# Optimization experiments

Hardware: AMD Instinct MI355X
Metric: run time of the kernel (lower is better)

The kernel has to match this reference:

```python
import jax, jax.numpy as jnp
import numpy as np

B, S, DM, H, HD = 2, 2048, 1024, 16, 64
MEM_SIZE = 1000
K_SIMILAR, K_CONTIG = 8, 2
K_TOTAL = K_SIMILAR + K_CONTIG  # 10 memory tokens
NEG = -1e9


def setup_inputs() -> dict:
    key = jax.random.key(0)
    k1, k2, k3, k4, k5, k6 = jax.random.split(key, 6)
    inputs = jax.random.normal(k1, (B, S, DM), dtype=jnp.float32)
    attention_mask = jnp.ones((B, S), dtype=jnp.float32)
    Wq = jax.random.normal(k2, (DM, H * HD), dtype=jnp.float32) * 0.02
    Wk = jax.random.normal(k3, (DM, H * HD), dtype=jnp.float32) * 0.02
    Wv = jax.random.normal(k4, (DM, H * HD), dtype=jnp.float32) * 0.02
    Wo = jax.random.normal(k5, (H * HD, DM), dtype=jnp.float32) * 0.02
    events = jax.random.normal(k6, (MEM_SIZE, H * HD), dtype=jnp.float32) * 0.02
    return {"inputs": inputs, "attention_mask": attention_mask,
            "Wq": Wq, "Wk": Wk, "Wv": Wv, "Wo": Wo, "events": events}


def _forward(inputs, attention_mask, Wq, Wk, Wv, Wo, events):
    # projections (no bias), split heads: [B, H, S, HD]
    q = (inputs @ Wq).reshape(B, S, H, HD).transpose(0, 2, 1, 3)
    k = (inputs @ Wk).reshape(B, S, H, HD).transpose(0, 2, 1, 3)
    v = (inputs @ Wv).reshape(B, S, H, HD).transpose(0, 2, 1, 3)

    # --- episodic retrieval: cosine top-k of last-token key vs events ---
    qvec = k[:, :, -1, :].reshape(B, H * HD)                       # [B, D]
    qn = qvec / (jnp.linalg.norm(qvec, axis=-1, keepdims=True) + 1e-8)
    en = events / (jnp.linalg.norm(events, axis=-1, keepdims=True) + 1e-8)
    sims = qn @ en.T                                               # [B, M]
    _, topk_idx = jax.lax.top_k(sims, K_TOTAL)                     # [B, K]
    retrieved = events[topk_idx]                                   # [B, K, D]
    retrieved_k = retrieved.reshape(B, K_TOTAL, H, HD).transpose(0, 2, 1, 3)  # [B,H,K,HD]
    retrieved_v = retrieved_k                                      # non-differential path

    aug_k = jnp.concatenate([retrieved_k, k], axis=2)              # [B,H,K+S,HD]
    aug_v = jnp.concatenate([retrieved_v, v], axis=2)

    # --- ALiBi bias: slopes * (pos_i - pos_j) on original cols, 0 on memory cols ---
    slopes = 2.0 ** (-8.0 * jnp.arange(1, H + 1, dtype=jnp.float32) / H)  # [H]
    positions = jnp.arange(S, dtype=jnp.float32)
    pos_diff = positions[:, None] - positions[None, :]             # [S, S]
    alibi = slopes[:, None, None] * pos_diff                       # [H, S, S]
    alibi = jnp.concatenate([jnp.zeros((H, S, K_TOTAL), jnp.float32), alibi], axis=-1)

    # --- causal mask: -1e9 strictly-upper on original cols, 0 on memory cols ---
    tri = jnp.where(jnp.arange(S)[None, :] > jnp.arange(S)[:, None], NEG, 0.0)  # [S,S]
    causal = jnp.concatenate([jnp.zeros((S, K_TOTAL), jnp.float32), tri], axis=-1)

    # --- padding mask: memory tokens always attendable ---
    aug_mask = jnp.concatenate([jnp.ones((B, K_TOTAL), jnp.float32), attention_mask], axis=-1)
    mask_bias = (1.0 - aug_mask)[:, None, None, :] * NEG           # [B,1,1,K+S]

    scores = jnp.einsum("bhqd,bhkd->bhqk", q, aug_k) / np.sqrt(HD)
    scores = scores + alibi[None] + causal[None, None] + mask_bias
    attn = jax.nn.softmax(scores, axis=-1)
    out = jnp.einsum("bhqk,bhkd->bhqd", attn, aug_v)               # [B,H,S,HD]
    out = out.transpose(0, 2, 1, 3).reshape(B, S, H * HD)
    return out @ Wo


def reference(inputs, attention_mask, Wq, Wk, Wv, Wo, events):
    return _forward(inputs, attention_mask, Wq, Wk, Wv, Wo, events)
```

## Files before the change

### kernel.cpp

```cpp
#include <hip/hip_runtime.h>
#include <hip/hip_bf16.h>
#include <math.h>

#define B_   2
#define S_   2048
#define DM_  1024
#define H_   16
#define HD_  64
#define MEM_ 1000
#define KTOT 10
#define NROW (B_ * S_)
#define NEG9 (-1e9f)
#define LDK  72
#define NITEMS 1024

typedef __attribute__((ext_vector_type(8))) short short8;
typedef __attribute__((ext_vector_type(4))) float f32x4;

__device__ __forceinline__ void gll16(const __hip_bfloat16* g, __hip_bfloat16* l) {
    __builtin_amdgcn_global_load_lds(
        (const __attribute__((address_space(1))) void*)g,
        (__attribute__((address_space(3))) void*)l, 16, 0, 0);
}

__global__ __launch_bounds__(256) void prep(const float* __restrict__ inputs,
                                            const float* __restrict__ Wq,
                                            const float* __restrict__ Wk,
                                            const float* __restrict__ Wv,
                                            const float* __restrict__ Wo,
                                            __hip_bfloat16* __restrict__ Ax,
                                            __hip_bfloat16* __restrict__ Wt,
                                            float* __restrict__ lk,
                                            int* __restrict__ ctr) {
    const int bx = blockIdx.x, tid = threadIdx.x;
    if (bx == 0 && tid == 0) *ctr = 0;

    if (bx < 2048) {
        const size_t i = ((size_t)bx * 256 + tid) * 8;
        float4 a = *(const float4*)&inputs[i];
        float4 b = *(const float4*)&inputs[i + 4];
        alignas(16) __hip_bfloat16 t[8];
        t[0] = __float2bfloat16(a.x); t[1] = __float2bfloat16(a.y);
        t[2] = __float2bfloat16(a.z); t[3] = __float2bfloat16(a.w);
        t[4] = __float2bfloat16(b.x); t[5] = __float2bfloat16(b.y);
        t[6] = __float2bfloat16(b.z); t[7] = __float2bfloat16(b.w);
        *(short8*)&Ax[i] = *(short8*)t;
        return;
    }
    if (bx < 3072) {
        const int idx = bx - 2048;
        const int g = idx >> 8, rem = idx & 255;
        const float* W = (g == 0) ? Wq : (g == 1) ? Wk : (g == 2) ? Wv : Wo;
        const int n0 = (rem & 15) * 64, k0 = (rem >> 4) * 64;
        __shared__ float T[64][65];
        {
            const int r = tid >> 4, c4 = (tid & 15) * 4;
#pragma unroll
            for (int p = 0; p < 4; ++p) {
                float4 v = *(const float4*)&W[(size_t)(k0 + r + p * 16) * 1024 + n0 + c4];
                T[r + p * 16][c4 + 0] = v.x; T[r + p * 16][c4 + 1] = v.y;
                T[r + p * 16][c4 + 2] = v.z; T[r + p * 16][c4 + 3] = v.w;
            }
        }
        __syncthreads();
        {
            const int n = tid >> 3, off = (tid & 7) * 8;
#pragma unroll
            for (int p = 0; p < 2; ++p) {
                const int nn = n + p * 32;
                alignas(16) __hip_bfloat16 t[8];
#pragma unroll
                for (int j = 0; j < 8; ++j) t[j] = __float2bfloat16(T[off + j][nn]);
                *(short8*)&Wt[((size_t)(g * 1024 + n0 + nn)) * 1024 + k0 + off] = *(short8*)t;
            }
        }
        return;
    }
    {
        const int idx = bx - 3072;
        const int xblk = idx & 15, b = idx >> 4;
        const int cl = tid & 63;
        const int col = xblk * 64 + cl;
        const int kq = tid >> 6;
        __shared__ float xr[1024];
        __shared__ float part[4][64];
        for (int i = tid; i < 1024; i += 256)
            xr[i] = inputs[((size_t)(b * S_ + S_ - 1)) * 1024 + i];
        __syncthreads();
        float acc = 0.f;
#pragma unroll 4
        for (int k = kq * 256; k < kq * 256 + 256; ++k)
            acc += xr[k] * Wk[(size_t)k * 1024 + col];
        part[kq][cl] = acc;
        __syncthreads();
        if (tid < 64)
            lk[b * 1024 + xblk * 64 + tid] =
                part[0][tid] + part[1][tid] + part[2][tid] + part[3][tid];
    }
}

__device__ __forceinline__ void store_out(__hip_bfloat16* p, float x) { *p = __float2bfloat16(x); }
__device__ __forceinline__ void store_out(float* p, float x) { *p = x; }

template <typename OutT>
__global__ __launch_bounds__(256) void gemm_mfma(const __hip_bfloat16* __restrict__ A,
                                                 const __hip_bfloat16* __restrict__ Bt,
                                                 OutT* __restrict__ C, int ldc) {
    __shared__ __hip_bfloat16 As[128 * 32];
    __shared__ __hip_bfloat16 Bs[128 * 32];
    const int tid = threadIdx.x;
    const int wave = tid >> 6, lane = tid & 63;
    const int quad = lane >> 4, lm = lane & 15;
    const int wr = wave >> 1, wc = wave & 1;
    const int m0 = blockIdx.y * 128, n0 = blockIdx.x * 128;

    const int r0 = tid >> 2, c0 = (tid & 3) * 8;
    const __hip_bfloat16* ga0 = &A[(size_t)(m0 + r0) * 1024 + c0];
    const __hip_bfloat16* ga1 = &A[(size_t)(m0 + 64 + r0) * 1024 + c0];
    const __hip_bfloat16* gb0 = &Bt[(size_t)(n0 + r0) * 1024 + c0];
    const __hip_bfloat16* gb1 = &Bt[(size_t)(n0 + 64 + r0) * 1024 + c0];
    __hip_bfloat16* la0 = &As[(wave * 64) * 8];
    __hip_bfloat16* la1 = &As[(256 + wave * 64) * 8];
    __hip_bfloat16* lb0 = &Bs[(wave * 64) * 8];
    __hip_bfloat16* lb1 = &Bs[(256 + wave * 64) * 8];

    f32x4 acc[4][4];
#pragma unroll
    for (int i = 0; i < 4; ++i)
#pragma unroll
        for (int j = 0; j < 4; ++j) acc[i][j] = (f32x4){0.f, 0.f, 0.f, 0.f};

    for (int k0 = 0; k0 < 1024; k0 += 32) {
        __syncthreads();
        gll16(ga0 + k0, la0);
        gll16(ga1 + k0, la1);
        gll16(gb0 + k0, lb0);
        gll16(gb1 + k0, lb1);
        __syncthreads();
        short8 af[4], bf4[4];
#pragma unroll
        for (int mt = 0; mt < 4; ++mt)
            af[mt] = *(const short8*)&As[(wr * 64 + mt * 16 + lm) * 32 + quad * 8];
#pragma unroll
        for (int nt = 0; nt < 4; ++nt)
            bf4[nt] = *(const short8*)&Bs[(wc * 64 + nt * 16 + lm) * 32 + quad * 8];
#pragma unroll
        for (int mt = 0; mt < 4; ++mt)
#pragma unroll
            for (int nt = 0; nt < 4; ++nt)
                acc[mt][nt] = __builtin_amdgcn_mfma_f32_16x16x32_bf16(
                    af[mt], bf4[nt], acc[mt][nt], 0, 0, 0);
    }
#pragma unroll
    for (int mt = 0; mt < 4; ++mt)
#pragma unroll
        for (int nt = 0; nt < 4; ++nt) {
            const int col = n0 + wc * 64 + nt * 16 + lm;
#pragma unroll
            for (int i = 0; i < 4; ++i) {
                const int row = m0 + wr * 64 + mt * 16 + quad * 4 + i;
                store_out(&C[(size_t)row * ldc + col], acc[mt][nt][i]);
            }
        }
}

__global__ __launch_bounds__(256) void sims_kernel(const float* __restrict__ lk,
                                                   const float* __restrict__ events,
                                                   float* __restrict__ sims) {
    const int b = blockIdx.y;
    const int tid = threadIdx.x;
    const int wave = tid >> 6, lane = tid & 63;
    __shared__ float qv[1024];
    for (int i = tid; i < 1024; i += 256)
        qv[i] = lk[b * 1024 + i];
    __syncthreads();

    const int m = blockIdx.x * 4 + wave;
    if (m >= MEM_) return;
    const float* ev = &events[(size_t)m * 1024];
    float dot = 0.f, nrm = 0.f;
    for (int d = lane; d < 1024; d += 64) {
        float e = ev[d];
        dot += qv[d] * e;
        nrm += e * e;
    }
    for (int off = 32; off; off >>= 1) {
        dot += __shfl_down(dot, off);
        nrm += __shfl_down(nrm, off);
    }
    if (lane == 0) sims[b * 1024 + m] = dot / (sqrtf(nrm) + 1e-8f);
}

__global__ __launch_bounds__(64) void topk10_kernel(const float* __restrict__ sims,
                                                    int* __restrict__ topk) {
    const int b = blockIdx.x;
    const int lane = threadIdx.x;
    const int base = lane * 16;
    float v[16];
#pragma unroll
    for (int j = 0; j < 16; ++j) {
        const int m = base + j;
        v[j] = (m < MEM_) ? sims[b * 1024 + m] : -INFINITY;
    }
    for (int it = 0; it < KTOT; ++it) {
        float best = -INFINITY; int bi = 0x7fffffff;
#pragma unroll
        for (int j = 0; j < 16; ++j)
            if (v[j] > best) { best = v[j]; bi = base + j; }
        for (int off = 32; off; off >>= 1) {
            const float ob = __shfl_xor(best, off);
            const int   oi = __shfl_xor(bi, off);
            if (ob > best || (ob == best && oi < bi)) { best = ob; bi = oi; }
        }
        if (lane == 0) topk[b * KTOT + it] = bi;
#pragma unroll
        for (int j = 0; j < 16; ++j)
            if (base + j == bi) v[j] = -INFINITY;
    }
}

__global__ __launch_bounds__(256) void attn_mfma(
        const __hip_bfloat16* __restrict__ qkv,
        const float* __restrict__ events,
        const int* __restrict__ topk,
        const float* __restrict__ amask,
        __hip_bfloat16* __restrict__ out,
        int* __restrict__ ctr) {
    const int tid = threadIdx.x;
    const int wave = tid >> 6, lane = tid & 63;
    const int quad = lane >> 4, lm = lane & 15;

    const __hip_bfloat16* qf = qkv;
    const __hip_bfloat16* kf = qkv + 1024;
    const __hip_bfloat16* vf = qkv + 2048;

    __shared__ __hip_bfloat16 Ks[64 * LDK];
    __shared__ __hip_bfloat16 Vt[80 * LDK];
    __shared__ __hip_bfloat16 Ps[64 * LDK];
    __shared__ float colb[64];
    __shared__ float redb[4];
    __shared__ int sItem;

    const int va = tid & 31, vdc = tid >> 5;
    const int vtok0 = va * 2, vd0 = vdc * 8;

    for (int i = tid; i < 16 * LDK; i += 256) {
        const int r = i / LDK;
        Vt[64 * LDK + i] = __float2bfloat16(r == 0 ? 1.0f : 0.0f);
    }

    for (;;) {
        __syncthreads();
        if (tid == 0) sItem = atomicAdd(ctr, 1);
        __syncthreads();
        const int n = sItem;
        if (n >= NITEMS) break;

        const int qt = 31 - (n >> 5);
        const int q0 = qt * 64;
        const int inner = n & 31;
        const int h = 15 - ((inner >> 1) & 15);
        const int b = inner & 1;
        const float slope = exp2f(-0.5f * (float)(h + 1));

        short8 qa[2];
        {
            const __hip_bfloat16* qsrc =
                &qf[((size_t)(b * S_ + q0 + wave * 16 + lm)) * 3072 + h * 64 + quad * 8];
            qa[0] = *(const short8*)qsrc;
            qa[1] = *(const short8*)(qsrc + 32);
        }
        for (int i = tid * 8; i < 64 * LDK; i += 256 * 8)
            *(int4*)&Vt[i] = make_int4(0, 0, 0, 0);
        __syncthreads();
        if (tid < 80) {
            const int tok = tid >> 3, d0 = (tid & 7) * 8;
            const int ev = topk[b * KTOT + tok];
            const float* es = &events[(size_t)ev * 1024 + h * 64 + d0];
#pragma unroll
            for (int j = 0; j < 8; ++j) {
                __hip_bfloat16 x = __float2bfloat16(es[j]);
                Ks[tok * LDK + d0 + j] = x;
                Vt[(d0 + j) * LDK + tok] = x;
            }
        }
        __syncthreads();

        float m_[4], mshift[4];
        f32x4 Oa[5];
#pragma unroll
        for (int i = 0; i < 4; ++i) {
            m_[i] = -INFINITY;
            mshift[i] = -slope * (float)(q0 + wave * 16 + quad * 4 + i);
        }
#pragma unroll
        for (int nt = 0; nt < 5; ++nt) Oa[nt] = (f32x4){0.f, 0.f, 0.f, 0.f};

        short8 pk[2], pv0, pv1;
        float pam = 1.f;
        auto prefetchKV = [&](int kt) {
            const __hip_bfloat16* ks = &kf[((size_t)(b * S_ + kt * 64)) * 3072 + h * 64];
#pragma unroll
            for (int u = 0; u < 2; ++u) {
                int c = tid * 2 + u, row = c >> 3, off = (c & 7) * 8;
                pk[u] = *(const short8*)&ks[(size_t)row * 3072 + off];
            }
            const __hip_bfloat16* v0 =
                &vf[((size_t)(b * S_ + kt * 64 + vtok0)) * 3072 + h * 64 + vd0];
            pv0 = *(const short8*)v0;
            pv1 = *(const short8*)(v0 + 3072);
            if (tid < 64) pam = amask[b * S_ + kt * 64 + tid];
        };
        auto stageKV = [&](int kt) {
#pragma unroll
            for (int u = 0; u < 2; ++u) {
                int c = tid * 2 + u, row = c >> 3, off = (c & 7) * 8;
                *(short8*)&Ks[row * LDK + off] = pk[u];
            }
#pragma unroll
            for (int j = 0; j < 8; ++j) {
                short2 pr; pr.x = pv0[j]; pr.y = pv1[j];
                *(short2*)&Vt[(vd0 + j) * LDK + vtok0] = pr;
            }
            if (tid < 64)
                colb[tid] = fmaf(-slope, (float)(kt * 64 + tid), (1.f - pam) * NEG9);
        };

        auto qk = [&](f32x4* sa) {
#pragma unroll
            for (int nt = 0; nt < 4; ++nt) sa[nt] = (f32x4){0.f, 0.f, 0.f, 0.f};
#pragma unroll
            for (int ks2 = 0; ks2 < 2; ++ks2) {
#pragma unroll
                for (int nt = 0; nt < 4; ++nt) {
                    short8 bk = *(const short8*)&Ks[(nt * 16 + lm) * LDK + ks2 * 32 + quad * 8];
                    sa[nt] = __builtin_amdgcn_mfma_f32_16x16x32_bf16(qa[ks2], bk, sa[nt], 0, 0, 0);
                }
            }
        };
        auto pv = [&]() {
#pragma unroll
            for (int ks2 = 0; ks2 < 2; ++ks2) {
                short8 ap = *(const short8*)&Ps[(wave * 16 + lm) * LDK + ks2 * 32 + quad * 8];
#pragma unroll
                for (int nt = 0; nt < 5; ++nt) {
                    short8 bv = *(const short8*)&Vt[(nt * 16 + lm) * LDK + ks2 * 32 + quad * 8];
                    Oa[nt] = __builtin_amdgcn_mfma_f32_16x16x32_bf16(ap, bv, Oa[nt], 0, 0, 0);
                }
            }
        };

        auto softmax_online = [&](const f32x4* sa, int kt, bool diag) {
            float cb[4];
            if (kt >= 0) {
#pragma unroll
                for (int nt = 0; nt < 4; ++nt) cb[nt] = colb[nt * 16 + lm];
            }
#pragma unroll
            for (int i = 0; i < 4; ++i) {
                const int lr = wave * 16 + quad * 4 + i;
                const int rg = q0 + lr;
                float s[4];
#pragma unroll
                for (int nt = 0; nt < 4; ++nt) {
                    const int cc = nt * 16 + lm;
                    if (kt < 0) {
                        s[nt] = (cc < KTOT) ? fmaf(sa[nt][i], 0.125f, mshift[i]) : NEG9;
                    } else {
                        float v = fmaf(sa[nt][i], 0.125f, cb[nt]);
                        s[nt] = (diag && kt * 64 + cc > rg) ? NEG9 : v;
                    }
                }
                float rmax = fmaxf(fmaxf(s[0], s[1]), fmaxf(s[2], s[3]));
#pragma unroll
                for (int off = 1; off < 16; off <<= 1)
                    rmax = fmaxf(rmax, __shfl_xor(rmax, off, 16));
                const float newm = fmaxf(m_[i], rmax);
                const float al = __expf(m_[i] - newm);
                m_[i] = newm;
#pragma unroll
                for (int nt = 0; nt < 4; ++nt)
                    Ps[lr * LDK + nt * 16 + lm] = __float2bfloat16(__expf(s[nt] - newm));
#pragma unroll
                for (int nt = 0; nt < 5; ++nt)
                    Oa[nt][i] *= al;
            }
        };

        auto softmax_fast = [&](const f32x4* sa, int cbase, bool diag) {
            float cb[4];
#pragma unroll
            for (int nt = 0; nt < 4; ++nt) cb[nt] = colb[nt * 16 + lm];
#pragma unroll
            for (int i = 0; i < 4; ++i) {
                const int lr = wave * 16 + quad * 4 + i;
                const float cm = m_[i];
                float p[4];
#pragma unroll
                for (int nt = 0; nt < 4; ++nt)
                    p[nt] = __expf(fmaf(sa[nt][i], 0.125f, cb[nt]) - cm);
                if (diag) {
                    const int rg = q0 + lr;
#pragma unroll
                    for (int nt = 0; nt < 4; ++nt)
                        if (cbase + nt * 16 + lm > rg) p[nt] = 0.f;
                }
#pragma unroll
                for (int nt = 0; nt < 4; ++nt)
                    Ps[lr * LDK + nt * 16 + lm] = __float2bfloat16(p[nt]);
            }
        };

        prefetchKV(0);
        {
            f32x4 sa[4];
            qk(sa);
            softmax_online(sa, -1, false);
            pv();
        }
        __syncthreads();
        stageKV(0);
        if (qt >= 1) prefetchKV(1);
        __syncthreads();
        {
            f32x4 sa[4];
            qk(sa);
            softmax_online(sa, 0, qt == 0);
            pv();
        }

        int ktend = 0;
        if (qt >= 1) {
            float mloc = fminf(fminf(m_[0], m_[1]), fminf(m_[2], m_[3]));
#pragma unroll
            for (int off = 1; off < 64; off <<= 1)
                mloc = fminf(mloc, __shfl_xor(mloc, off, 64));
            if (lane == 0) redb[wave] = mloc;
            __syncthreads();
            const float mmin = fminf(fminf(redb[0], redb[1]), fminf(redb[2], redb[3]));
            ktend = min(qt, (int)((118.f - mmin) / (64.f * slope)));
        }
        for (int kt = 1; kt <= ktend; ++kt) {
            __syncthreads();
            stageKV(kt);
            if (kt < ktend) prefetchKV(kt + 1);
            __syncthreads();
            f32x4 sa[4];
            qk(sa);
            softmax_fast(sa, kt * 64, kt == qt);
            pv();
        }

#pragma unroll
        for (int i = 0; i < 4; ++i) {
            const int lr = wave * 16 + quad * 4 + i;
            const float l = __shfl(Oa[4][i], (lane & 48));
            const float inv = 1.f / l;
            __hip_bfloat16* dst = &out[((size_t)(b * S_ + q0 + lr)) * 1024 + h * 64 + lm];
#pragma unroll
            for (int nt = 0; nt < 4; ++nt)
                dst[nt * 16] = __float2bfloat16(Oa[nt][i] * inv);
        }
    }
}

extern "C" void kernel_launch(void* const* d_in, const int* in_sizes, int n_in,
                              void* d_out, int out_size, void* d_ws, size_t ws_size,
                              hipStream_t stream) {
    const float* inputs = (const float*)d_in[0];
    const float* amask  = (const float*)d_in[1];
    const float* Wq     = (const float*)d_in[2];
    const float* Wk     = (const float*)d_in[3];
    const float* Wv     = (const float*)d_in[4];
    const float* Wo     = (const float*)d_in[5];
    const float* events = (const float*)d_in[6];
    float* out = (float*)d_out;

    __hip_bfloat16* Ax  = (__hip_bfloat16*)d_ws;
    __hip_bfloat16* Wt  = Ax + (size_t)NROW * 1024;
    __hip_bfloat16* qkv = Wt + (size_t)4096 * 1024;
    __hip_bfloat16* ao  = qkv + (size_t)NROW * 3072;
    float* lk   = (float*)(ao + (size_t)NROW * 1024);
    float* sims = lk + 2 * 1024;
    int* topk   = (int*)(sims + 2 * 1024);
    int* ctr    = topk + B_ * KTOT;

    dim3 blk(256);
    prep<<<3104, blk, 0, stream>>>(inputs, Wq, Wk, Wv, Wo, Ax, Wt, lk, ctr);
    sims_kernel<<<dim3(250, B_), blk, 0, stream>>>(lk, events, sims);
    topk10_kernel<<<B_, 64, 0, stream>>>(sims, topk);
    gemm_mfma<__hip_bfloat16><<<dim3(24, 32), blk, 0, stream>>>(Ax, Wt, qkv, 3072);
    attn_mfma<<<768, blk, 0, stream>>>(qkv, events, topk, amask, ao, ctr);
    gemm_mfma<float><<<dim3(8, 32), blk, 0, stream>>>(
        ao, Wt + (size_t)3072 * 1024, out, 1024);
}
```

Before: 244.2 us.

## Double-buffer attention K/V tiles, defer PV, and fuse top-k into sims kernel

The attention loop now uses two LDS buffers for K and V^T. The P·V MFMA for the previous tile is issued after the QK MFMAs of the current tile, before the current softmax, so work from neighbouring tiles can overlap. Separately, the top-10 selection moves into the similarity kernel through a last-block-done atomic counter, which removes one kernel launch. The cost is more LDS per block, which may reduce occupancy, plus an extra atomic and fence in each sims block.

```diff
diff --git a/kernel.cpp b/kernel.cpp
--- a/kernel.cpp
+++ b/kernel.cpp
@@ -33,7 +33,7 @@
                                             float* __restrict__ lk,
                                             int* __restrict__ ctr) {
     const int bx = blockIdx.x, tid = threadIdx.x;
-    if (bx == 0 && tid == 0) *ctr = 0;
+    if (bx == 0 && tid == 0) { ctr[0] = 0; ctr[1] = 0; }
 
     if (bx < 2048) {
         const size_t i = ((size_t)bx * 256 + tid) * 8;
@@ -164,19 +164,21 @@
         }
 }
 
-__global__ __launch_bounds__(256) void sims_kernel(const float* __restrict__ lk,
-                                                   const float* __restrict__ events,
-                                                   float* __restrict__ sims) {
+__global__ __launch_bounds__(256) void sims_topk(const float* __restrict__ lk,
+                                                 const float* __restrict__ events,
+                                                 float* __restrict__ sims,
+                                                 int* __restrict__ topk,
+                                                 int* __restrict__ done) {
     const int b = blockIdx.y;
     const int tid = threadIdx.x;
     const int wave = tid >> 6, lane = tid & 63;
     __shared__ float qv[1024];
+    __shared__ int sLast;
     for (int i = tid; i < 1024; i += 256)
         qv[i] = lk[b * 1024 + i];
     __syncthreads();
 
     const int m = blockIdx.x * 4 + wave;
-    if (m >= MEM_) return;
     const float* ev = &events[(size_t)m * 1024];
     float dot = 0.f, nrm = 0.f;
     for (int d = lane; d < 1024; d += 64) {
@@ -189,33 +191,35 @@
         nrm += __shfl_down(nrm, off);
     }
     if (lane == 0) sims[b * 1024 + m] = dot / (sqrtf(nrm) + 1e-8f);
-}
-
-__global__ __launch_bounds__(64) void topk10_kernel(const float* __restrict__ sims,
-                                                    int* __restrict__ topk) {
-    const int b = blockIdx.x;
-    const int lane = threadIdx.x;
-    const int base = lane * 16;
-    float v[16];
-#pragma unroll
-    for (int j = 0; j < 16; ++j) {
-        const int m = base + j;
-        v[j] = (m < MEM_) ? sims[b * 1024 + m] : -INFINITY;
-    }
-    for (int it = 0; it < KTOT; ++it) {
-        float best = -INFINITY; int bi = 0x7fffffff;
-#pragma unroll
-        for (int j = 0; j < 16; ++j)
-            if (v[j] > best) { best = v[j]; bi = base + j; }
-        for (int off = 32; off; off >>= 1) {
-            const float ob = __shfl_xor(best, off);
-            const int   oi = __shfl_xor(bi, off);
-            if (ob > best || (ob == best && oi < bi)) { best = ob; bi = oi; }
-        }
-        if (lane == 0) topk[b * KTOT + it] = bi;
-#pragma unroll
-        for (int j = 0; j < 16; ++j)
-            if (base + j == bi) v[j] = -INFINITY;
+
+    __threadfence();
+    if (tid == 0) sLast = (atomicAdd(done, 1) == 499) ? 1 : 0;
+    __syncthreads();
+    if (!sLast) return;
+    const int w = wave;
+    if (w < 2) {
+        const int base = lane * 16;
+        float v[16];
+#pragma unroll
+        for (int j = 0; j < 16; ++j) {
+            const int mm = base + j;
+            v[j] = (mm < MEM_) ? sims[w * 1024 + mm] : -INFINITY;
+        }
+        for (int it = 0; it < KTOT; ++it) {
+            float best = -INFINITY; int bi = 0x7fffffff;
+#pragma unroll
+            for (int j = 0; j < 16; ++j)
+                if (v[j] > best) { best = v[j]; bi = base + j; }
+            for (int off = 32; off; off >>= 1) {
+                const float ob = __shfl_xor(best, off);
+                const int   oi = __shfl_xor(bi, off);
+                if (ob > best || (ob == best && oi < bi)) { best = ob; bi = oi; }
+            }
+            if (lane == 0) topk[w * KTOT + it] = bi;
+#pragma unroll
+            for (int j = 0; j < 16; ++j)
+                if (base + j == bi) v[j] = -INFINITY;
+        }
     }
 }
 
@@ -234,8 +238,8 @@
     const __hip_bfloat16* kf = qkv + 1024;
     const __hip_bfloat16* vf = qkv + 2048;
 
-    __shared__ __hip_bfloat16 Ks[64 * LDK];
-    __shared__ __hip_bfloat16 Vt[80 * LDK];
+    __shared__ __hip_bfloat16 Ks[2][64 * LDK];
+    __shared__ __hip_bfloat16 Vt[2][80 * LDK];
     __shared__ __hip_bfloat16 Ps[64 * LDK];
     __shared__ float colb[64];
     __shared__ float redb[4];
@@ -246,7 +250,9 @@
 
     for (int i = tid; i < 16 * LDK; i += 256) {
         const int r = i / LDK;
-        Vt[64 * LDK + i] = __float2bfloat16(r == 0 ? 1.0f : 0.0f);
+        const __hip_bfloat16 x = __float2bfloat16(r == 0 ? 1.0f : 0.0f);
+        Vt[0][64 * LDK + i] = x;
+        Vt[1][64 * LDK + i] = x;
     }
 
     for (;;) {
@@ -271,7 +277,7 @@
             qa[1] = *(const short8*)(qsrc + 32);
         }
         for (int i = tid * 8; i < 64 * LDK; i += 256 * 8)
-            *(int4*)&Vt[i] = make_int4(0, 0, 0, 0);
+            *(int4*)&Vt[0][i] = make_int4(0, 0, 0, 0);
         __syncthreads();
         if (tid < 80) {
             const int tok = tid >> 3, d0 = (tid & 7) * 8;
@@ -280,8 +286,8 @@
 #pragma unroll
             for (int j = 0; j < 8; ++j) {
                 __hip_bfloat16 x = __float2bfloat16(es[j]);
-                Ks[tok * LDK + d0 + j] = x;
-                Vt[(d0 + j) * LDK + tok] = x;
+                Ks[0][tok * LDK + d0 + j] = x;
+                Vt[0][(d0 + j) * LDK + tok] = x;
             }
         }
         __syncthreads();
@@ -311,40 +317,40 @@
             pv1 = *(const short8*)(v0 + 3072);
             if (tid < 64) pam = amask[b * S_ + kt * 64 + tid];
         };
-        auto stageKV = [&](int kt) {
+        auto stageKV = [&](int kt, int buf) {
 #pragma unroll
             for (int u = 0; u < 2; ++u) {
                 int c = tid * 2 + u, row = c >> 3, off = (c & 7) * 8;
-                *(short8*)&Ks[row * LDK + off] = pk[u];
+                *(short8*)&Ks[buf][row * LDK + off] = pk[u];
             }
 #pragma unroll
             for (int j = 0; j < 8; ++j) {
                 short2 pr; pr.x = pv0[j]; pr.y = pv1[j];
-                *(short2*)&Vt[(vd0 + j) * LDK + vtok0] = pr;
+                *(short2*)&Vt[buf][(vd0 + j) * LDK + vtok0] = pr;
             }
             if (tid < 64)
                 colb[tid] = fmaf(-slope, (float)(kt * 64 + tid), (1.f - pam) * NEG9);
         };
 
-        auto qk = [&](f32x4* sa) {
+        auto qk = [&](f32x4* sa, int buf) {
 #pragma unroll
             for (int nt = 0; nt < 4; ++nt) sa[nt] = (f32x4){0.f, 0.f, 0.f, 0.f};
 #pragma unroll
             for (int ks2 = 0; ks2 < 2; ++ks2) {
 #pragma unroll
                 for (int nt = 0; nt < 4; ++nt) {
-                    short8 bk = *(const short8*)&Ks[(nt * 16 + lm) * LDK + ks2 * 32 + quad * 8];
+                    short8 bk = *(const short8*)&Ks[buf][(nt * 16 + lm) * LDK + ks2 * 32 + quad * 8];
                     sa[nt] = __builtin_amdgcn_mfma_f32_16x16x32_bf16(qa[ks2], bk, sa[nt], 0, 0, 0);
                 }
             }
         };
-        auto pv = [&]() {
+        auto pv = [&](int buf) {
 #pragma unroll
             for (int ks2 = 0; ks2 < 2; ++ks2) {
                 short8 ap = *(const short8*)&Ps[(wave * 16 + lm) * LDK + ks2 * 32 + quad * 8];
 #pragma unroll
                 for (int nt = 0; nt < 5; ++nt) {
-                    short8 bv = *(const short8*)&Vt[(nt * 16 + lm) * LDK + ks2 * 32 + quad * 8];
+                    short8 bv = *(const short8*)&Vt[buf][(nt * 16 + lm) * LDK + ks2 * 32 + quad * 8];
                     Oa[nt] = __builtin_amdgcn_mfma_f32_16x16x32_bf16(ap, bv, Oa[nt], 0, 0, 0);
                 }
             }
@@ -414,19 +420,19 @@
         prefetchKV(0);
         {
             f32x4 sa[4];
-            qk(sa);
+            qk(sa, 0);
             softmax_online(sa, -1, false);
-            pv();
-        }
-        __syncthreads();
-        stageKV(0);
+            pv(0);
+        }
+        __syncthreads();
+        stageKV(0, 1);
         if (qt >= 1) prefetchKV(1);
         __syncthreads();
         {
             f32x4 sa[4];
-            qk(sa);
+            qk(sa, 1);
             softmax_online(sa, 0, qt == 0);
-            pv();
+            pv(1);
         }
 
         int ktend = 0;
@@ -439,16 +445,27 @@
             __syncthreads();
             const float mmin = fminf(fminf(redb[0], redb[1]), fminf(redb[2], redb[3]));
             ktend = min(qt, (int)((118.f - mmin) / (64.f * slope)));
-        }
-        for (int kt = 1; kt <= ktend; ++kt) {
+            if (ktend < 1) ktend = 0;
+        }
+
+        if (ktend >= 1) {
+            f32x4 sa[4];
+            stageKV(1, 0);
+            if (ktend >= 2) prefetchKV(2);
             __syncthreads();
-            stageKV(kt);
-            if (kt < ktend) prefetchKV(kt + 1);
-            __syncthreads();
-            f32x4 sa[4];
-            qk(sa);
-            softmax_fast(sa, kt * 64, kt == qt);
-            pv();
+            qk(sa, 0);
+            softmax_fast(sa, 64, 1 == qt);
+            for (int kt = 2; kt <= ktend; ++kt) {
+                const int buf = (kt + 1) & 1;
+                __syncthreads();
+                stageKV(kt, buf);
+                if (kt < ktend) prefetchKV(kt + 1);
+                __syncthreads();
+                qk(sa, buf);
+                pv(1 - buf);
+                softmax_fast(sa, kt * 64, kt == qt);
+            }
+            pv((ktend + 1) & 1);
         }
 
 #pragma unroll
@@ -487,8 +504,7 @@
 
     dim3 blk(256);
     prep<<<3104, blk, 0, stream>>>(inputs, Wq, Wk, Wv, Wo, Ax, Wt, lk, ctr);
-    sims_kernel<<<dim3(250, B_), blk, 0, stream>>>(lk, events, sims);
-    topk10_kernel<<<B_, 64, 0, stream>>>(sims, topk);
+    sims_topk<<<dim3(250, B_), blk, 0, stream>>>(lk, events, sims, topk, ctr + 1);
     gemm_mfma<__hip_bfloat16><<<dim3(24, 32), blk, 0, stream>>>(Ax, Wt, qkv, 3072);
     attn_mfma<<<768, blk, 0, stream>>>(qkv, events, topk, amask, ao, ctr);
     gemm_mfma<float><<<dim3(8, 32), blk, 0, stream>>>(
```

Measured after the change: 276.2 us. 13.1% more time.

## Fuse output projection into persistent attention kernel via band-ready counters

Applied to the files above, without the earlier changes.

The Wo output-projection GEMM becomes extra work items in the persistent attention kernel. Each GEMM tile spins on a per-band counter until the 32 attention items covering its 128 rows have written their output, which lets the projection overlap the attention tail. The top-k kernel is folded into the similarity kernel using a last-block-done atomic. These remove two launches and the serialization between attention and projection, at the cost of spin-waiting and reliance on forward-progress ordering of the work-steal counter.

```diff
diff --git a/kernel.cpp b/kernel.cpp
--- a/kernel.cpp
+++ b/kernel.cpp
@@ -12,7 +12,9 @@
 #define NROW (B_ * S_)
 #define NEG9 (-1e9f)
 #define LDK  72
-#define NITEMS 1024
+#define NATT 1024
+#define NGEMM 256
+#define NITEMS_T (NATT + NGEMM)
 
 typedef __attribute__((ext_vector_type(8))) short short8;
 typedef __attribute__((ext_vector_type(4))) float f32x4;
@@ -33,7 +35,7 @@
                                             float* __restrict__ lk,
                                             int* __restrict__ ctr) {
     const int bx = blockIdx.x, tid = threadIdx.x;
-    if (bx == 0 && tid == 0) *ctr = 0;
+    if (bx == 0 && tid < 34) ctr[tid] = 0;
 
     if (bx < 2048) {
         const size_t i = ((size_t)bx * 256 + tid) * 8;
@@ -99,13 +101,9 @@
     }
 }
 
-__device__ __forceinline__ void store_out(__hip_bfloat16* p, float x) { *p = __float2bfloat16(x); }
-__device__ __forceinline__ void store_out(float* p, float x) { *p = x; }
-
-template <typename OutT>
 __global__ __launch_bounds__(256) void gemm_mfma(const __hip_bfloat16* __restrict__ A,
                                                  const __hip_bfloat16* __restrict__ Bt,
-                                                 OutT* __restrict__ C, int ldc) {
+                                                 __hip_bfloat16* __restrict__ C, int ldc) {
     __shared__ __hip_bfloat16 As[128 * 32];
     __shared__ __hip_bfloat16 Bs[128 * 32];
     const int tid = threadIdx.x;
@@ -159,24 +157,26 @@
 #pragma unroll
             for (int i = 0; i < 4; ++i) {
                 const int row = m0 + wr * 64 + mt * 16 + quad * 4 + i;
-                store_out(&C[(size_t)row * ldc + col], acc[mt][nt][i]);
+                C[(size_t)row * ldc + col] = __float2bfloat16(acc[mt][nt][i]);
             }
         }
 }
 
-__global__ __launch_bounds__(256) void sims_kernel(const float* __restrict__ lk,
-                                                   const float* __restrict__ events,
-                                                   float* __restrict__ sims) {
+__global__ __launch_bounds__(256) void sims_topk(const float* __restrict__ lk,
+                                                 const float* __restrict__ events,
+                                                 float* __restrict__ sims,
+                                                 int* __restrict__ topk,
+                                                 int* __restrict__ done) {
     const int b = blockIdx.y;
     const int tid = threadIdx.x;
     const int wave = tid >> 6, lane = tid & 63;
     __shared__ float qv[1024];
+    __shared__ int sLast;
     for (int i = tid; i < 1024; i += 256)
         qv[i] = lk[b * 1024 + i];
     __syncthreads();
 
     const int m = blockIdx.x * 4 + wave;
-    if (m >= MEM_) return;
     const float* ev = &events[(size_t)m * 1024];
     float dot = 0.f, nrm = 0.f;
     for (int d = lane; d < 1024; d += 64) {
@@ -189,42 +189,46 @@
         nrm += __shfl_down(nrm, off);
     }
     if (lane == 0) sims[b * 1024 + m] = dot / (sqrtf(nrm) + 1e-8f);
+
+    __threadfence();
+    if (tid == 0) sLast = (atomicAdd(done, 1) == 499) ? 1 : 0;
+    __syncthreads();
+    if (!sLast) return;
+    const int w = wave;
+    if (w < 2) {
+        const int base = lane * 16;
+        float v[16];
+#pragma unroll
+        for (int j = 0; j < 16; ++j) {
+            const int mm = base + j;
+            v[j] = (mm < MEM_) ? sims[w * 1024 + mm] : -INFINITY;
+        }
+        for (int it = 0; it < KTOT; ++it) {
+            float best = -INFINITY; int bi = 0x7fffffff;
+#pragma unroll
+            for (int j = 0; j < 16; ++j)
+                if (v[j] > best) { best = v[j]; bi = base + j; }
+            for (int off = 32; off; off >>= 1) {
+                const float ob = __shfl_xor(best, off);
+                const int   oi = __shfl_xor(bi, off);
+                if (ob > best || (ob == best && oi < bi)) { best = ob; bi = oi; }
+            }
+            if (lane == 0) topk[w * KTOT + it] = bi;
+#pragma unroll
+            for (int j = 0; j < 16; ++j)
+                if (base + j == bi) v[j] = -INFINITY;
+        }
+    }
 }
 
-__global__ __launch_bounds__(64) void topk10_kernel(const float* __restrict__ sims,
-                                                    int* __restrict__ topk) {
-    const int b = blockIdx.x;
-    const int lane = threadIdx.x;
-    const int base = lane * 16;
-    float v[16];
-#pragma unroll
-    for (int j = 0; j < 16; ++j) {
-        const int m = base + j;
-        v[j] = (m < MEM_) ? sims[b * 1024 + m] : -INFINITY;
-    }
-    for (int it = 0; it < KTOT; ++it) {
-        float best = -INFINITY; int bi = 0x7fffffff;
-#pragma unroll
-        for (int j = 0; j < 16; ++j)
-            if (v[j] > best) { best = v[j]; bi = base + j; }
-        for (int off = 32; off; off >>= 1) {
-            const float ob = __shfl_xor(best, off);
-            const int   oi = __shfl_xor(bi, off);
-            if (ob > best || (ob == best && oi < bi)) { best = ob; bi = oi; }
-        }
-        if (lane == 0) topk[b * KTOT + it] = bi;
-#pragma unroll
-        for (int j = 0; j < 16; ++j)
-            if (base + j == bi) v[j] = -INFINITY;
-    }
-}
-
-__global__ __launch_bounds__(256) void attn_mfma(
+__global__ __launch_bounds__(256) void attn_fused(
         const __hip_bfloat16* __restrict__ qkv,
         const float* __restrict__ events,
         const int* __restrict__ topk,
         const float* __restrict__ amask,
-        __hip_bfloat16* __restrict__ out,
+        __hip_bfloat16* __restrict__ ao,
+        const __hip_bfloat16* __restrict__ WtO,
+        float* __restrict__ out,
         int* __restrict__ ctr) {
     const int tid = threadIdx.x;
     const int wave = tid >> 6, lane = tid & 63;
@@ -241,6 +245,9 @@
     __shared__ float redb[4];
     __shared__ int sItem;
 
+    int* steal = ctr;
+    int* bandctr = ctr + 2;
+
     const int va = tid & 31, vdc = tid >> 5;
     const int vtok0 = va * 2, vd0 = vdc * 8;
 
@@ -251,10 +258,78 @@
 
     for (;;) {
         __syncthreads();
-        if (tid == 0) sItem = atomicAdd(ctr, 1);
+        if (tid == 0) sItem = atomicAdd(steal, 1);
         __syncthreads();
         const int n = sItem;
-        if (n >= NITEMS) break;
+        if (n >= NITEMS_T) break;
+
+        if (n >= NATT) {
+            const int g = n - NATT;
+            const int qp = 15 - (g >> 4);
+            const int inner = g & 15;
+            const int bb = inner >> 3, ni = inner & 7;
+            const int band = bb * 16 + qp;
+            if (tid == 0) {
+                while (atomicAdd(&bandctr[band], 0) < 32)
+                    __builtin_amdgcn_s_sleep(8);
+            }
+            __syncthreads();
+            __threadfence();
+
+            const int wr = wave >> 1, wc = wave & 1;
+            const int m0 = band * 128, n0 = ni * 128;
+            const int r0 = tid >> 2, c0 = (tid & 3) * 8;
+            const __hip_bfloat16* ga0 = &ao[(size_t)(m0 + r0) * 1024 + c0];
+            const __hip_bfloat16* ga1 = &ao[(size_t)(m0 + 64 + r0) * 1024 + c0];
+            const __hip_bfloat16* gb0 = &WtO[(size_t)(n0 + r0) * 1024 + c0];
+            const __hip_bfloat16* gb1 = &WtO[(size_t)(n0 + 64 + r0) * 1024 + c0];
+            __hip_bfloat16* AsL = &Ks[0];
+            __hip_bfloat16* BsL = &Ps[0];
+            __hip_bfloat16* la0 = &AsL[(wave * 64) * 8];
+            __hip_bfloat16* la1 = &AsL[(256 + wave * 64) * 8];
+            __hip_bfloat16* lb0 = &BsL[(wave * 64) * 8];
+            __hip_bfloat16* lb1 = &BsL[(256 + wave * 64) * 8];
+
+            f32x4 acc[4][4];
+#pragma unroll
+            for (int i = 0; i < 4; ++i)
+#pragma unroll
+                for (int j = 0; j < 4; ++j) acc[i][j] = (f32x4){0.f, 0.f, 0.f, 0.f};
+
+            for (int k0 = 0; k0 < 1024; k0 += 32) {
+                __syncthreads();
+                gll16(ga0 + k0, la0);
+                gll16(ga1 + k0, la1);
+                gll16(gb0 + k0, lb0);
+                gll16(gb1 + k0, lb1);
+                __syncthreads();
+                short8 af[4], bf4[4];
+#pragma unroll
+                for (int mt = 0; mt < 4; ++mt)
+                    af[mt] = *(const short8*)&AsL[(wr * 64 + mt * 16 + lm) * 32 + quad * 8];
+#pragma unroll
+                for (int nt = 0; nt < 4; ++nt)
+                    bf4[nt] = *(const short8*)&BsL[(wc * 64 + nt * 16 + lm) * 32 + quad * 8];
+#pragma unroll
+                for (int mt = 0; mt < 4; ++mt)
+#pragma unroll
+                    for (int nt = 0; nt < 4; ++nt)
+                        acc[mt][nt] = __builtin_amdgcn_mfma_f32_16x16x32_bf16(
+                            af[mt], bf4[nt], acc[mt][nt], 0, 0, 0);
+            }
+#pragma unroll
+            for (int mt = 0; mt < 4; ++mt)
+#pragma unroll
+                for (int nt = 0; nt < 4; ++nt) {
+                    const int col = n0 + wc * 64 + nt * 16 + lm;
+#pragma unroll
+                    for (int i = 0; i < 4; ++i) {
+                        const int row = m0 + wr * 64 + mt * 16 + quad * 4 + i;
+                        out[(size_t)row * 1024 + col] = acc[mt][nt][i];
+                    }
+                }
+            continue;
+        }
 
         const int qt = 31 - (n >> 5);
         const int q0 = qt * 64;
@@ -456,11 +531,15 @@
             const int lr = wave * 16 + quad * 4 + i;
             const float l = __shfl(Oa[4][i], (lane & 48));
             const float inv = 1.f / l;
-            __hip_bfloat16* dst = &out[((size_t)(b * S_ + q0 + lr)) * 1024 + h * 64 + lm];
+            __hip_bfloat16* dst = &ao[((size_t)(b * S_ + q0 + lr)) * 1024 + h * 64 + lm];
 #pragma unroll
             for (int nt = 0; nt < 4; ++nt)
                 dst[nt * 16] = __float2bfloat16(Oa[nt][i] * inv);
         }
+
+        __syncthreads();
+        __threadfence();
+        if (tid == 0) atomicAdd(&bandctr[b * 16 + (qt >> 1)], 1);
     }
 }
 
@@ -487,10 +566,8 @@
 
     dim3 blk(256);
     prep<<<3104, blk, 0, stream>>>(inputs, Wq, Wk, Wv, Wo, Ax, Wt, lk, ctr);
-    sims_kernel<<<dim3(250, B_), blk, 0, stream>>>(lk, events, sims);
-    topk10_kernel<<<B_, 64, 0, stream>>>(sims, topk);
-    gemm_mfma<__hip_bfloat16><<<dim3(24, 32), blk, 0, stream>>>(Ax, Wt, qkv, 3072);
-    attn_mfma<<<768, blk, 0, stream>>>(qkv, events, topk, amask, ao, ctr);
-    gemm_mfma<float><<<dim3(8, 32), blk, 0, stream>>>(
-        ao, Wt + (size_t)3072 * 1024, out, 1024);
+    sims_topk<<<dim3(250, B_), blk, 0, stream>>>(lk, events, sims, topk, ctr + 1);
+    gemm_mfma<<<dim3(24, 32), blk, 0, stream>>>(Ax, Wt, qkv, 3072);
+    attn_fused<<<768, blk, 0, stream>>>(qkv, events, topk, amask, ao,
+                                        Wt + (size_t)3072 * 1024, out, ctr);
 }
```

New measurement: 408.6 us. 1.67x slower.
